# Kernel optimization log

Measured on AMD Instinct MI355X. Metric: run time of the kernel, lower is better.

## Reference

```python
import jax, jax.numpy as jnp
import numpy as np

B, N, DIM, H, DH = 2, 2048, 256, 8, 32
DIM_INNER = H * DH  # 256


def setup_inputs() -> dict:
    key = jax.random.key(0)
    ks = jax.random.split(key, 8)
    s = DIM ** -0.5  # keep activations / logits in a sane range
    return {
        "x_real": jax.random.normal(ks[0], (B, N, DIM), jnp.float32),
        "x_imag": jax.random.normal(ks[1], (B, N, DIM), jnp.float32),
        "wq_r": jax.random.normal(ks[2], (DIM, DIM_INNER), jnp.float32) * s,
        "wq_i": jax.random.normal(ks[3], (DIM, DIM_INNER), jnp.float32) * s,
        "wkv_r": jax.random.normal(ks[4], (DIM, 2 * DIM_INNER), jnp.float32) * s,
        "wkv_i": jax.random.normal(ks[5], (DIM, 2 * DIM_INNER), jnp.float32) * s,
        "wo_r": jax.random.normal(ks[6], (DIM_INNER, DIM), jnp.float32) * s,
        "wo_i": jax.random.normal(ks[7], (DIM_INNER, DIM), jnp.float32) * s,
    }


def _clin(xr, xi, wr, wi):
    # complex linear: (xr + i xi) @ (wr + i wi)
    return xr @ wr - xi @ wi, xr @ wi + xi @ wr


def _split_heads(t):
    b, n, _ = t.shape
    return t.reshape(b, n, H, DH).transpose(0, 2, 1, 3)  # b h n d


def _merge_heads(t):
    b, h, n, d = t.shape
    return t.transpose(0, 2, 1, 3).reshape(b, n, h * d)


def reference(x_real, x_imag, wq_r, wq_i, wkv_r, wkv_i, wo_r, wo_i):
    # complex projections
    qr, qi = _clin(x_real, x_imag, wq_r, wq_i)
    kvr, kvi = _clin(x_real, x_imag, wkv_r, wkv_i)
    kr, vr = jnp.split(kvr, 2, axis=-1)
    ki, vi = jnp.split(kvi, 2, axis=-1)
    qr, qi, kr, ki, vr, vi = map(_split_heads, (qr, qi, kr, ki, vr, vi))

    # complex_attention_complete (sec 3.2 eq 3): 4 real SDPA replicas.
    # q repeat '(c r b)' -> blocks [qr, qr, qi, qi]; k repeat '(r c b)' -> [kr, ki, kr, ki]
    scale = DH ** -0.5
    Q = jnp.stack([qr, qr, qi, qi])        # [4, b, h, n, d]
    K = jnp.stack([kr, ki, kr, ki])
    sim = jnp.einsum('rbhid,rbhjd->rbhij', Q, K) * scale
    A = jax.nn.softmax(sim, axis=-1)       # [4, b, h, n, n]

    av = lambda a, v: jnp.einsum('bhij,bhjd->bhid', a, v)
    # sign-recombine trick: indices [0,3,5,6 | 1,2,4,7], sign [[1,-1,-1,-1],[1,1,1,-1]]
    o_r = av(A[0], vr) - av(A[1], vi) - av(A[2], vi) - av(A[3], vr)
    o_i = av(A[0], vi) + av(A[1], vr) + av(A[2], vr) - av(A[3], vi)

    mr, mi = _merge_heads(o_r), _merge_heads(o_i)
    out_r, out_i = _clin(mr, mi, wo_r, wo_i)
    # real view of the complex output: [b, n, dim, 2]
    return jnp.stack([out_r, out_i], axis=-1)
```

## Files before the change

kernel.cpp:

```cpp
#include <hip/hip_runtime.h>
#include <math.h>

namespace {
constexpr int kB = 2, kN = 2048, kDim = 256, kH = 8, kDH = 32;
constexpr int kBH = kB * kH;
constexpr long kPlane = (long)kBH * kN * kDH;
constexpr float kQScaleL2 = 0.25506852552f;
}

typedef unsigned short u16;
typedef short short8 __attribute__((ext_vector_type(8)));
typedef short short4v __attribute__((ext_vector_type(4)));
typedef float floatx16 __attribute__((ext_vector_type(16)));
#define MFMA_BF16(a, b, c) __builtin_amdgcn_mfma_f32_32x32x16_bf16(a, b, c, 0, 0, 0)

__device__ inline u16 bf16b(float x) {
    union { float f; unsigned u; } c; c.f = x;
    unsigned r = c.u + 0x7FFFu + ((c.u >> 16) & 1u);
    return (u16)(r >> 16);
}
__device__ inline unsigned pack2(float x, float y) {
    return (unsigned)bf16b(x) | ((unsigned)bf16b(y) << 16);
}
__device__ inline unsigned packtr(float lo, float hi) {
    return __builtin_amdgcn_perm(__float_as_uint(hi), __float_as_uint(lo), 0x07060302u);
}
__device__ inline short8 mk8(const float* e) {
    union { unsigned u[4]; short8 s; } c;
    c.u[0] = packtr(e[0], e[1]);
    c.u[1] = packtr(e[2], e[3]);
    c.u[2] = packtr(e[4], e[5]);
    c.u[3] = packtr(e[6], e[7]);
    return c.s;
}
__device__ inline void gload16(const u16* g, u16* l) {
    __builtin_amdgcn_global_load_lds(
        (const __attribute__((address_space(1))) void*)g,
        (__attribute__((address_space(3))) void*)l, 16, 0, 0);
}

__global__ __launch_bounds__(256, 2) void prep_w(
    const float* __restrict__ xr_g, const float* __restrict__ xi_g,
    const float* __restrict__ wq_r, const float* __restrict__ wq_i,
    const float* __restrict__ wkv_r, const float* __restrict__ wkv_i,
    const float* __restrict__ wo_r, const float* __restrict__ wo_i,
    u16* __restrict__ Wbig, u16* __restrict__ WoT, u16* __restrict__ Xbf)
{
    const int T = blockIdx.x;
    const int tid = threadIdx.x;

    if (T < 256) {
        __shared__ __align__(16) u16 tile[64 * 68];
        const float* src;
        float sgn;
        int stride, colbase, kt, dt;
        bool isWo = false;
        int g = 0, ri = 0, hi;
        if (T < 192) {
            const int p = T >> 4, q = T & 15;
            kt = (q >> 2) * 64; dt = (q & 3) * 64;
            g = p >> 1; hi = p & 1;
            if (g < 2) {
                stride = 256; colbase = dt;
                if (g == 0) { src = hi ? wq_i : wq_r; sgn = hi ? -kQScaleL2 : kQScaleL2; }
                else        { src = hi ? wq_r : wq_i; sgn = kQScaleL2; }
            } else {
                stride = 512; colbase = dt + ((g >= 4) ? 256 : 0);
                if ((g & 1) == 0) { src = hi ? wkv_i : wkv_r; sgn = hi ? -1.f : 1.f; }
                else              { src = hi ? wkv_r : wkv_i; sgn = 1.f; }
            }
        } else {
            isWo = true;
            const int pp = T - 192;
            const int qd = pp >> 4, q = pp & 15;
            ri = qd & 1; hi = qd >> 1;
            kt = (q >> 2) * 64; dt = (q & 3) * 64;
            stride = 256; colbase = dt;
            if (ri == 0) { src = hi ? wo_i : wo_r; sgn = hi ? -1.f : 1.f; }
            else         { src = hi ? wo_r : wo_i; sgn = 1.f; }
        }

        const int ti = tid >> 4, tj = tid & 15;
        #pragma unroll
        for (int rr = 0; rr < 4; ++rr) {
            const int krel = ti + rr * 16;
            const float4 f = *(const float4*)(src + (long)(kt + krel) * stride
                                              + colbase + tj * 4);
            tile[(tj * 4 + 0) * 68 + krel] = bf16b(f.x * sgn);
            tile[(tj * 4 + 1) * 68 + krel] = bf16b(f.y * sgn);
            tile[(tj * 4 + 2) * 68 + krel] = bf16b(f.z * sgn);
            tile[(tj * 4 + 3) * 68 + krel] = bf16b(f.w * sgn);
        }
        __syncthreads();

        const int di = tid >> 4, kj = tid & 15;
        #pragma unroll
        for (int dr = 0; dr < 4; ++dr) {
            const int dd = di + dr * 16;
            const short4v v = *(const short4v*)(tile + dd * 68 + kj * 4);
            long idx;
            if (!isWo) idx = (long)(g * 256 + dt + dd) * 512 + hi * 256 + kt + kj * 4;
            else       idx = (long)(2 * (dt + dd) + ri) * 512 + hi * 256 + kt + kj * 4;
            *(short4v*)(((!isWo) ? Wbig : WoT) + idx) = v;
        }
    } else {
        const long o = ((long)(T - 256) * 256 + tid) * 4;
        const int row = (int)(o >> 9);
        const int col = (int)(o & 511);
        const float* src = (col < 256) ? (xr_g + (long)row * 256 + col)
                                       : (xi_g + (long)row * 256 + col - 256);
        const float4 f = *(const float4*)src;
        short4v v;
        v[0] = (short)bf16b(f.x); v[1] = (short)bf16b(f.y);
        v[2] = (short)bf16b(f.z); v[3] = (short)bf16b(f.w);
        *(short4v*)(Xbf + o) = v;
    }
}

__global__ __launch_bounds__(256, 2) void gemm_proj(
    const u16* __restrict__ Xbf, const u16* __restrict__ BT,
    u16* __restrict__ qr, u16* __restrict__ qi, u16* __restrict__ kr,
    u16* __restrict__ ki, u16* __restrict__ vrT, u16* __restrict__ viT)
{
    __shared__ __align__(16) u16 sA[2][128 * 32];
    __shared__ __align__(16) u16 sB[2][128 * 32];
    const int tid = threadIdx.x;
    const int lane = tid & 63, l31 = lane & 31, lh = lane >> 5;
    const int w = tid >> 6, wrow = w & 1, wcol = w >> 1;
    const int n0 = blockIdx.x * 128, m0 = blockIdx.y * 128;

    const int rb0 = w * 32;
    const int grow = lane >> 2;
    const int gseg = (lane & 3) * 8;

    auto stage = [&](int b, int kt) {
        #pragma unroll
        for (int half = 0; half < 2; ++half) {
            const int r = rb0 + half * 16;
            gload16(Xbf + (long)(m0 + r + grow) * 512 + kt + gseg, &sA[b][r * 32]);
            gload16(BT + (long)(n0 + r + grow) * 512 + kt + gseg, &sB[b][r * 32]);
        }
    };

    floatx16 a00 = {0}, a01 = {0}, a10 = {0}, a11 = {0};
    stage(0, 0);
    for (int it = 0; it < 16; ++it) {
        const int cur = it & 1;
        __syncthreads();
        if (it < 15) stage(cur ^ 1, (it + 1) * 32);
        #pragma unroll
        for (int s = 0; s < 2; ++s) {
            const int ko = s * 16 + lh * 8;
            const short8 fa0 = *(const short8*)(&sA[cur][(wrow * 64 + l31) * 32 + ko]);
            const short8 fa1 = *(const short8*)(&sA[cur][(wrow * 64 + 32 + l31) * 32 + ko]);
            const short8 fb0 = *(const short8*)(&sB[cur][(wcol * 64 + l31) * 32 + ko]);
            const short8 fb1 = *(const short8*)(&sB[cur][(wcol * 64 + 32 + l31) * 32 + ko]);
            a00 = MFMA_BF16(fa0, fb0, a00);
            a01 = MFMA_BF16(fa0, fb1, a01);
            a10 = MFMA_BF16(fa1, fb0, a10);
            a11 = MFMA_BF16(fa1, fb1, a11);
        }
    }

    __syncthreads();
    u16* scr = ((u16*)sA) + w * 1088;

    floatx16 accs[2][2] = {{a00, a01}, {a10, a11}};
    #pragma unroll
    for (int rt = 0; rt < 2; ++rt) {
        #pragma unroll
        for (int ct = 0; ct < 2; ++ct) {
            const int colb = n0 + wcol * 64 + ct * 32;
            const int g = colb >> 8;
            const int h = (colb & 255) >> 5;
            if (g < 4) {
                u16* pl = (g == 0) ? qr : (g == 1) ? qi : (g == 2) ? kr : ki;
                #pragma unroll
                for (int reg = 0; reg < 16; ++reg) {
                    const int row = m0 + wrow * 64 + rt * 32 + (reg & 3) + 8 * (reg >> 2) + 4 * lh;
                    const int b = row >> 11, nn = row & 2047;
                    pl[(((long)(b * 8 + h)) * 2048 + nn) * 32 + l31] = bf16b(accs[rt][ct][reg]);
                }
            } else {
                #pragma unroll
                for (int q = 0; q < 4; ++q) {
                    union { unsigned u[2]; uint2 v; } pk;
                    pk.u[0] = pack2(accs[rt][ct][4 * q + 0], accs[rt][ct][4 * q + 1]);
                    pk.u[1] = pack2(accs[rt][ct][4 * q + 2], accs[rt][ct][4 * q + 3]);
                    *(uint2*)(scr + l31 * 34 + 8 * q + 4 * lh) = pk.v;
                }
                asm volatile("s_waitcnt lgkmcnt(0)" ::: "memory");
                const int rowb = m0 + wrow * 64 + rt * 32;
                const int b_ = rowb >> 11, nnb = rowb & 2047;
                u16* plane = (g == 4) ? vrT : viT;
                u16* rowbase = plane + ((long)(b_ * 8 + h) * 32) * 2048 + nnb;
                const int p = lane & 15;
                const int sp = (p & ~6) | ((p & 2) << 1) | ((p & 4) >> 1);
                const int dgrp = lane >> 4;
                #pragma unroll
                for (int ds_ = 0; ds_ < 8; ++ds_) {
                    const int d = ds_ * 4 + dgrp;
                    const unsigned v = *(const unsigned*)(scr + d * 34 + 2 * sp);
                    *(unsigned*)(rowbase + (long)d * 2048 + 2 * p) = v;
                }
                asm volatile("s_waitcnt lgkmcnt(0)" ::: "memory");
            }
        }
    }
}

__global__ __launch_bounds__(256, 2) void attn_kernel(
    const u16* __restrict__ qr_g, const u16* __restrict__ qi_g,
    const u16* __restrict__ kr_g, const u16* __restrict__ ki_g,
    const u16* __restrict__ vrT_g, const u16* __restrict__ viT_g,
    u16* __restrict__ xo)
{
    __shared__ __align__(16) u16 smem[2][2][64 * 40];

    const int tid = threadIdx.x;
    const int lane = tid & 63, l31 = lane & 31, lh = lane >> 5;
    const int w = tid >> 6, strip = w & 1, qtype = w >> 1;
    const int bh = blockIdx.x;
    const int i0 = blockIdx.y * 64;
    const long base = (long)bh * kN * kDH;

    const u16* qg = (qtype ? qi_g : qr_g) + base;
    short8 qB0, qB1;
    {
        const u16* qp = qg + (long)(i0 + strip * 32 + l31) * kDH;
        qB0 = *(const short8*)(qp + lh * 8);
        qB1 = *(const short8*)(qp + 16 + lh * 8);
    }

    const int srow = tid & 63;
    const int sseg = tid >> 6;
    const u16* kptr = ((srow < 32) ? kr_g : ki_g) + base
                    + (long)(srow & 31) * kDH + sseg * 8;
    const u16* vptr = ((srow < 32) ? vrT_g : viT_g)
                    + ((long)bh * 32 + (srow & 31)) * kN + sseg * 8;

    short8 kreg = *(const short8*)kptr;
    short8 vreg = *(const short8*)vptr;

    floatx16 U0r = {0}, U0i = {0}, U1r = {0}, U1i = {0};
    float La0 = 0.f, La1 = 0.f;

    for (int t = 0; t < 64; ++t) {
        u16* bK = smem[0][t & 1];
        u16* bV = smem[1][t & 1];
        *(short8*)(bK + srow * 40 + sseg * 8) = kreg;
        *(short8*)(bV + srow * 40 + sseg * 8) = vreg;
        __syncthreads();
        if (t < 63) {
            kreg = *(const short8*)(kptr + (long)(t + 1) * 1024);
            vreg = *(const short8*)(vptr + (t + 1) * 32);
        }

        const short8 ka0 = *(const short8*)(bK + l31 * 40 + lh * 8);
        const short8 ka1 = *(const short8*)(bK + l31 * 40 + 16 + lh * 8);
        const short8 kb0 = *(const short8*)(bK + (32 + l31) * 40 + lh * 8);
        const short8 kb1 = *(const short8*)(bK + (32 + l31) * 40 + 16 + lh * 8);
        floatx16 S0 = {0}, S1 = {0};
        S0 = MFMA_BF16(ka0, qB0, S0);
        S0 = MFMA_BF16(ka1, qB1, S0);
        S1 = MFMA_BF16(kb0, qB0, S1);
        S1 = MFMA_BF16(kb1, qB1, S1);

        float e0[16], e1[16];
        #pragma unroll
        for (int r = 0; r < 16; ++r) {
            e0[r] = __builtin_amdgcn_exp2f(S0[r]);
            La0 += e0[r];
        }
        #pragma unroll
        for (int r = 0; r < 16; ++r) {
            e1[r] = __builtin_amdgcn_exp2f(S1[r]);
            La1 += e1[r];
        }
        const short8 F0a = mk8(&e0[0]);
        const short8 F0b = mk8(&e0[8]);
        const short8 F1a = mk8(&e1[0]);
        const short8 F1b = mk8(&e1[8]);

        const short8 va0 = *(const short8*)(bV + l31 * 40 + lh * 8);
        const short8 va1 = *(const short8*)(bV + l31 * 40 + 16 + lh * 8);
        const short8 vb0 = *(const short8*)(bV + (32 + l31) * 40 + lh * 8);
        const short8 vb1 = *(const short8*)(bV + (32 + l31) * 40 + 16 + lh * 8);

        U0r = MFMA_BF16(va0, F0a, U0r);
        U0r = MFMA_BF16(va1, F0b, U0r);
        U0i = MFMA_BF16(vb0, F0a, U0i);
        U0i = MFMA_BF16(vb1, F0b, U0i);
        U1r = MFMA_BF16(va0, F1a, U1r);
        U1r = MFMA_BF16(va1, F1b, U1r);
        U1i = MFMA_BF16(vb0, F1a, U1i);
        U1i = MFMA_BF16(vb1, F1b, U1i);
    }

    La0 += __shfl_xor(La0, 32);
    La1 += __shfl_xor(La1, 32);
    const float iL0 = 1.f / La0, iL1 = 1.f / La1;

    float po_r[16], po_i[16];
    #pragma unroll
    for (int r = 0; r < 16; ++r) {
        if (qtype == 0) {
            po_r[r] =  U0r[r] * iL0 - U1i[r] * iL1;
            po_i[r] =  U0i[r] * iL0 + U1r[r] * iL1;
        } else {
            po_r[r] = -U0i[r] * iL0 - U1r[r] * iL1;
            po_i[r] =  U0r[r] * iL0 - U1i[r] * iL1;
        }
    }

    __syncthreads();
    float* sC = (float*)smem;
    if (qtype == 1) {
        float* dst = sC + strip * (2 * 32 * 33);
        #pragma unroll
        for (int r = 0; r < 16; ++r) {
            const int d = (r & 3) + 8 * (r >> 2) + 4 * lh;
            dst[d * 33 + l31] = po_r[r];
            dst[32 * 33 + d * 33 + l31] = po_i[r];
        }
    }
    __syncthreads();
    if (qtype == 0) {
        const float* src = sC + strip * (2 * 32 * 33);
        const int b = bh >> 3, h = bh & 7;
        u16* xrow = xo + ((long)(b * 2048 + i0 + strip * 32 + l31)) * 512 + h * 32;
        #pragma unroll
        for (int g = 0; g < 4; ++g) {
            const int d0 = 8 * g + 4 * lh;
            union { unsigned u[2]; uint2 v; } pr, pi;
            pr.u[0] = pack2(po_r[4 * g + 0] + src[(d0 + 0) * 33 + l31],
                            po_r[4 * g + 1] + src[(d0 + 1) * 33 + l31]);
            pr.u[1] = pack2(po_r[4 * g + 2] + src[(d0 + 2) * 33 + l31],
                            po_r[4 * g + 3] + src[(d0 + 3) * 33 + l31]);
            pi.u[0] = pack2(po_i[4 * g + 0] + src[32 * 33 + (d0 + 0) * 33 + l31],
                            po_i[4 * g + 1] + src[32 * 33 + (d0 + 1) * 33 + l31]);
            pi.u[1] = pack2(po_i[4 * g + 2] + src[32 * 33 + (d0 + 2) * 33 + l31],
                            po_i[4 * g + 3] + src[32 * 33 + (d0 + 3) * 33 + l31]);
            *(uint2*)(xrow + d0) = pr.v;
            *(uint2*)(xrow + 256 + d0) = pi.v;
        }
    }
}

__global__ __launch_bounds__(256, 2) void gemm_oproj(
    const u16* __restrict__ Xo, const u16* __restrict__ BT, float* __restrict__ out)
{
    __shared__ __align__(16) u16 sA[2][64 * 32];
    __shared__ __align__(16) u16 sB[2][64 * 32];
    const int tid = threadIdx.x;
    const int lane = tid & 63, l31 = lane & 31, lh = lane >> 5;
    const int w = tid >> 6, wrow = w & 1, wcol = w >> 1;
    const int n0 = blockIdx.x * 64, m0 = blockIdx.y * 64;

    const int rb0 = w * 16;
    const int grow = lane >> 2;
    const int gseg = (lane & 3) * 8;

    auto stage = [&](int b, int kt) {
        gload16(Xo + (long)(m0 + rb0 + grow) * 512 + kt + gseg, &sA[b][rb0 * 32]);
        gload16(BT + (long)(n0 + rb0 + grow) * 512 + kt + gseg, &sB[b][rb0 * 32]);
    };

    floatx16 acc = {0};
    stage(0, 0);
    for (int it = 0; it < 16; ++it) {
        const int cur = it & 1;
        __syncthreads();
        if (it < 15) stage(cur ^ 1, (it + 1) * 32);
        #pragma unroll
        for (int s = 0; s < 2; ++s) {
            const int ko = s * 16 + lh * 8;
            const short8 fa = *(const short8*)(&sA[cur][(wrow * 32 + l31) * 32 + ko]);
            const short8 fb = *(const short8*)(&sB[cur][(wcol * 32 + l31) * 32 + ko]);
            acc = MFMA_BF16(fa, fb, acc);
        }
    }

    const int col = n0 + wcol * 32 + l31;
    #pragma unroll
    for (int reg = 0; reg < 16; ++reg) {
        const int row = m0 + wrow * 32 + (reg & 3) + 8 * (reg >> 2) + 4 * lh;
        out[(long)row * 512 + col] = acc[reg];
    }
}

extern "C" void kernel_launch(void* const* d_in, const int* in_sizes, int n_in,
                              void* d_out, int out_size, void* d_ws, size_t ws_size,
                              hipStream_t stream) {
    const float* xr    = (const float*)d_in[0];
    const float* xi    = (const float*)d_in[1];
    const float* wq_r  = (const float*)d_in[2];
    const float* wq_i  = (const float*)d_in[3];
    const float* wkv_r = (const float*)d_in[4];
    const float* wkv_i = (const float*)d_in[5];
    const float* wo_r  = (const float*)d_in[6];
    const float* wo_i  = (const float*)d_in[7];
    float* out = (float*)d_out;

    u16* ws16 = (u16*)d_ws;
    u16* qr   = ws16 + 0 * kPlane;
    u16* qi   = ws16 + 1 * kPlane;
    u16* kr   = ws16 + 2 * kPlane;
    u16* ki   = ws16 + 3 * kPlane;
    u16* vrT  = ws16 + 4 * kPlane;
    u16* viT  = ws16 + 5 * kPlane;
    u16* xo   = ws16 + 6 * kPlane;
    u16* Wbig = ws16 + 8 * kPlane;
    u16* WoT  = Wbig + 786432;
    u16* Xbf  = xo;

    prep_w<<<2304, 256, 0, stream>>>(xr, xi, wq_r, wq_i, wkv_r, wkv_i, wo_r, wo_i,
                                     Wbig, WoT, Xbf);
    gemm_proj<<<dim3(12, 32), 256, 0, stream>>>(Xbf, Wbig, qr, qi, kr, ki, vrT, viT);
    attn_kernel<<<dim3(kBH, kN / 64), 256, 0, stream>>>(qr, qi, kr, ki, vrT, viT, xo);
    gemm_oproj<<<dim3(8, 64), 256, 0, stream>>>(xo, WoT, out);
}
```

Measured before the change: 162.9 us.

## Software-pipeline PV MFMAs one iteration behind QK with triple-buffered V tiles

The P·V matrix multiplies for tile t-1 now issue right after the QK^T MFMAs of tile t, before that tile's exp2 work, so matrix-core and VALU work can overlap within a wave. V shared-memory tiles become triple-buffered so the previous tile's V is still intact while the next one is being written. A tail block after the loop handles the last tile's P·V. The cost is more shared memory and extra live registers for the carried probability fragments and V operands, which may put pressure on the two-blocks-per-CU occupancy target.

```diff
diff --git a/kernel.cpp b/kernel.cpp
--- a/kernel.cpp
+++ b/kernel.cpp
@@ -215,7 +215,7 @@
     const u16* __restrict__ vrT_g, const u16* __restrict__ viT_g,
     u16* __restrict__ xo)
 {
-    __shared__ __align__(16) u16 smem[2][2][64 * 40];
+    __shared__ __align__(16) u16 smem[5 * 2560];
 
     const int tid = threadIdx.x;
     const int lane = tid & 63, l31 = lane & 31, lh = lane >> 5;
@@ -244,16 +244,28 @@
 
     floatx16 U0r = {0}, U0i = {0}, U1r = {0}, U1i = {0};
     float La0 = 0.f, La1 = 0.f;
-
+    short8 pF0a, pF0b, pF1a, pF1b;
+
+    int vb = 0;
     for (int t = 0; t < 64; ++t) {
-        u16* bK = smem[0][t & 1];
-        u16* bV = smem[1][t & 1];
+        u16* bK = smem + (t & 1) * 2560;
+        u16* bV = smem + (2 + vb) * 2560;
+        const int vbp = vb ? vb - 1 : 2;
+        const u16* bVp = smem + (2 + vbp) * 2560;
         *(short8*)(bK + srow * 40 + sseg * 8) = kreg;
         *(short8*)(bV + srow * 40 + sseg * 8) = vreg;
         __syncthreads();
         if (t < 63) {
             kreg = *(const short8*)(kptr + (long)(t + 1) * 1024);
             vreg = *(const short8*)(vptr + (t + 1) * 32);
+        }
+
+        short8 va0, va1, vb0, vb1;
+        if (t) {
+            va0 = *(const short8*)(bVp + l31 * 40 + lh * 8);
+            va1 = *(const short8*)(bVp + l31 * 40 + 16 + lh * 8);
+            vb0 = *(const short8*)(bVp + (32 + l31) * 40 + lh * 8);
+            vb1 = *(const short8*)(bVp + (32 + l31) * 40 + 16 + lh * 8);
         }
 
         const short8 ka0 = *(const short8*)(bK + l31 * 40 + lh * 8);
@@ -266,6 +278,17 @@
         S1 = MFMA_BF16(kb0, qB0, S1);
         S1 = MFMA_BF16(kb1, qB1, S1);
 
+        if (t) {
+            U0r = MFMA_BF16(va0, pF0a, U0r);
+            U0r = MFMA_BF16(va1, pF0b, U0r);
+            U0i = MFMA_BF16(vb0, pF0a, U0i);
+            U0i = MFMA_BF16(vb1, pF0b, U0i);
+            U1r = MFMA_BF16(va0, pF1a, U1r);
+            U1r = MFMA_BF16(va1, pF1b, U1r);
+            U1i = MFMA_BF16(vb0, pF1a, U1i);
+            U1i = MFMA_BF16(vb1, pF1b, U1i);
+        }
+
         float e0[16], e1[16];
         #pragma unroll
         for (int r = 0; r < 16; ++r) {
@@ -277,24 +300,28 @@
             e1[r] = __builtin_amdgcn_exp2f(S1[r]);
             La1 += e1[r];
         }
-        const short8 F0a = mk8(&e0[0]);
-        const short8 F0b = mk8(&e0[8]);
-        const short8 F1a = mk8(&e1[0]);
-        const short8 F1b = mk8(&e1[8]);
-
-        const short8 va0 = *(const short8*)(bV + l31 * 40 + lh * 8);
-        const short8 va1 = *(const short8*)(bV + l31 * 40 + 16 + lh * 8);
-        const short8 vb0 = *(const short8*)(bV + (32 + l31) * 40 + lh * 8);
-        const short8 vb1 = *(const short8*)(bV + (32 + l31) * 40 + 16 + lh * 8);
-
-        U0r = MFMA_BF16(va0, F0a, U0r);
-        U0r = MFMA_BF16(va1, F0b, U0r);
-        U0i = MFMA_BF16(vb0, F0a, U0i);
-        U0i = MFMA_BF16(vb1, F0b, U0i);
-        U1r = MFMA_BF16(va0, F1a, U1r);
-        U1r = MFMA_BF16(va1, F1b, U1r);
-        U1i = MFMA_BF16(vb0, F1a, U1i);
-        U1i = MFMA_BF16(vb1, F1b, U1i);
+        pF0a = mk8(&e0[0]);
+        pF0b = mk8(&e0[8]);
+        pF1a = mk8(&e1[0]);
+        pF1b = mk8(&e1[8]);
+
+        vb = (vb == 2) ? 0 : vb + 1;
+    }
+
+    {
+        const u16* bVp = smem + 2 * 2560;
+        const short8 va0 = *(const short8*)(bVp + l31 * 40 + lh * 8);
+        const short8 va1 = *(const short8*)(bVp + l31 * 40 + 16 + lh * 8);
+        const short8 vb0 = *(const short8*)(bVp + (32 + l31) * 40 + lh * 8);
+        const short8 vb1 = *(const short8*)(bVp + (32 + l31) * 40 + 16 + lh * 8);
+        U0r = MFMA_BF16(va0, pF0a, U0r);
+        U0r = MFMA_BF16(va1, pF0b, U0r);
+        U0i = MFMA_BF16(vb0, pF0a, U0i);
+        U0i = MFMA_BF16(vb1, pF0b, U0i);
+        U1r = MFMA_BF16(va0, pF1a, U1r);
+        U1r = MFMA_BF16(va1, pF1b, U1r);
+        U1i = MFMA_BF16(vb0, pF1a, U1i);
+        U1i = MFMA_BF16(vb1, pF1b, U1i);
     }
 
     La0 += __shfl_xor(La0, 32);
```

Result: no change. 164.5 us (+1.0%).

## Process two query strips per wave in attention to reuse K/V fragments

Applied to the files above, without the earlier changes.

Each attention block now runs 2 waves instead of 4. Each wave handles both 32-row query strips, so the K and V fragments read from LDS are reused across two strips, and the staging loads per thread double. This halves the LDS fragment reads per unit of MFMA work and the number of barrier participants. The cost is roughly twice the accumulator registers per wave, which could lower occupancy or cause spills, and fewer waves are available per block to hide latency.

```diff
diff --git a/kernel.cpp b/kernel.cpp
--- a/kernel.cpp
+++ b/kernel.cpp
@@ -209,7 +209,7 @@
     }
 }
 
-__global__ __launch_bounds__(256, 2) void attn_kernel(
+__global__ __launch_bounds__(128, 2) void attn_kernel(
     const u16* __restrict__ qr_g, const u16* __restrict__ qi_g,
     const u16* __restrict__ kr_g, const u16* __restrict__ ki_g,
     const u16* __restrict__ vrT_g, const u16* __restrict__ viT_g,
@@ -219,130 +219,187 @@
 
     const int tid = threadIdx.x;
     const int lane = tid & 63, l31 = lane & 31, lh = lane >> 5;
-    const int w = tid >> 6, strip = w & 1, qtype = w >> 1;
+    const int qtype = tid >> 6;
     const int bh = blockIdx.x;
     const int i0 = blockIdx.y * 64;
     const long base = (long)bh * kN * kDH;
 
     const u16* qg = (qtype ? qi_g : qr_g) + base;
-    short8 qB0, qB1;
+    short8 qA0, qA1, qB0, qB1;
     {
-        const u16* qp = qg + (long)(i0 + strip * 32 + l31) * kDH;
-        qB0 = *(const short8*)(qp + lh * 8);
-        qB1 = *(const short8*)(qp + 16 + lh * 8);
+        const u16* qpA = qg + (long)(i0 + l31) * kDH;
+        qA0 = *(const short8*)(qpA + lh * 8);
+        qA1 = *(const short8*)(qpA + 16 + lh * 8);
+        const u16* qpB = qg + (long)(i0 + 32 + l31) * kDH;
+        qB0 = *(const short8*)(qpB + lh * 8);
+        qB1 = *(const short8*)(qpB + 16 + lh * 8);
     }
 
     const int srow = tid & 63;
-    const int sseg = tid >> 6;
+    const int sseg = (tid >> 6) * 16;
     const u16* kptr = ((srow < 32) ? kr_g : ki_g) + base
-                    + (long)(srow & 31) * kDH + sseg * 8;
+                    + (long)(srow & 31) * kDH + sseg;
     const u16* vptr = ((srow < 32) ? vrT_g : viT_g)
-                    + ((long)bh * 32 + (srow & 31)) * kN + sseg * 8;
-
-    short8 kreg = *(const short8*)kptr;
-    short8 vreg = *(const short8*)vptr;
-
-    floatx16 U0r = {0}, U0i = {0}, U1r = {0}, U1i = {0};
-    float La0 = 0.f, La1 = 0.f;
+                    + ((long)bh * 32 + (srow & 31)) * kN + sseg;
+
+    short8 k0 = *(const short8*)kptr;
+    short8 k1 = *(const short8*)(kptr + 8);
+    short8 v0 = *(const short8*)vptr;
+    short8 v1 = *(const short8*)(vptr + 8);
+
+    floatx16 UA0r = {0}, UA0i = {0}, UA1r = {0}, UA1i = {0};
+    floatx16 UB0r = {0}, UB0i = {0}, UB1r = {0}, UB1i = {0};
+    float LaA0 = 0.f, LaA1 = 0.f, LaB0 = 0.f, LaB1 = 0.f;
 
     for (int t = 0; t < 64; ++t) {
         u16* bK = smem[0][t & 1];
         u16* bV = smem[1][t & 1];
-        *(short8*)(bK + srow * 40 + sseg * 8) = kreg;
-        *(short8*)(bV + srow * 40 + sseg * 8) = vreg;
+        *(short8*)(bK + srow * 40 + sseg) = k0;
+        *(short8*)(bK + srow * 40 + sseg + 8) = k1;
+        *(short8*)(bV + srow * 40 + sseg) = v0;
+        *(short8*)(bV + srow * 40 + sseg + 8) = v1;
         __syncthreads();
         if (t < 63) {
-            kreg = *(const short8*)(kptr + (long)(t + 1) * 1024);
-            vreg = *(const short8*)(vptr + (t + 1) * 32);
+            k0 = *(const short8*)(kptr + (long)(t + 1) * 1024);
+            k1 = *(const short8*)(kptr + (long)(t + 1) * 1024 + 8);
+            v0 = *(const short8*)(vptr + (t + 1) * 32);
+            v1 = *(const short8*)(vptr + (t + 1) * 32 + 8);
         }
 
         const short8 ka0 = *(const short8*)(bK + l31 * 40 + lh * 8);
         const short8 ka1 = *(const short8*)(bK + l31 * 40 + 16 + lh * 8);
         const short8 kb0 = *(const short8*)(bK + (32 + l31) * 40 + lh * 8);
         const short8 kb1 = *(const short8*)(bK + (32 + l31) * 40 + 16 + lh * 8);
-        floatx16 S0 = {0}, S1 = {0};
-        S0 = MFMA_BF16(ka0, qB0, S0);
-        S0 = MFMA_BF16(ka1, qB1, S0);
-        S1 = MFMA_BF16(kb0, qB0, S1);
-        S1 = MFMA_BF16(kb1, qB1, S1);
-
-        float e0[16], e1[16];
-        #pragma unroll
-        for (int r = 0; r < 16; ++r) {
-            e0[r] = __builtin_amdgcn_exp2f(S0[r]);
-            La0 += e0[r];
-        }
-        #pragma unroll
-        for (int r = 0; r < 16; ++r) {
-            e1[r] = __builtin_amdgcn_exp2f(S1[r]);
-            La1 += e1[r];
-        }
-        const short8 F0a = mk8(&e0[0]);
-        const short8 F0b = mk8(&e0[8]);
-        const short8 F1a = mk8(&e1[0]);
-        const short8 F1b = mk8(&e1[8]);
+
+        short8 FA0a, FA0b, FA1a, FA1b;
+        {
+            floatx16 S0 = {0}, S1 = {0};
+            S0 = MFMA_BF16(ka0, qA0, S0);
+            S0 = MFMA_BF16(ka1, qA1, S0);
+            S1 = MFMA_BF16(kb0, qA0, S1);
+            S1 = MFMA_BF16(kb1, qA1, S1);
+            float e0[16], e1[16];
+            #pragma unroll
+            for (int r = 0; r < 16; ++r) {
+                e0[r] = __builtin_amdgcn_exp2f(S0[r]);
+                LaA0 += e0[r];
+            }
+            #pragma unroll
+            for (int r = 0; r < 16; ++r) {
+                e1[r] = __builtin_amdgcn_exp2f(S1[r]);
+                LaA1 += e1[r];
+            }
+            FA0a = mk8(&e0[0]); FA0b = mk8(&e0[8]);
+            FA1a = mk8(&e1[0]); FA1b = mk8(&e1[8]);
+        }
+
+        short8 FB0a, FB0b, FB1a, FB1b;
+        {
+            floatx16 S0 = {0}, S1 = {0};
+            S0 = MFMA_BF16(ka0, qB0, S0);
+            S0 = MFMA_BF16(ka1, qB1, S0);
+            S1 = MFMA_BF16(kb0, qB0, S1);
+            S1 = MFMA_BF16(kb1, qB1, S1);
+            float e0[16], e1[16];
+            #pragma unroll
+            for (int r = 0; r < 16; ++r) {
+                e0[r] = __builtin_amdgcn_exp2f(S0[r]);
+                LaB0 += e0[r];
+            }
+            #pragma unroll
+            for (int r = 0; r < 16; ++r) {
+                e1[r] = __builtin_amdgcn_exp2f(S1[r]);
+                LaB1 += e1[r];
+            }
+            FB0a = mk8(&e0[0]); FB0b = mk8(&e0[8]);
+            FB1a = mk8(&e1[0]); FB1b = mk8(&e1[8]);
+        }
 
         const short8 va0 = *(const short8*)(bV + l31 * 40 + lh * 8);
         const short8 va1 = *(const short8*)(bV + l31 * 40 + 16 + lh * 8);
         const short8 vb0 = *(const short8*)(bV + (32 + l31) * 40 + lh * 8);
         const short8 vb1 = *(const short8*)(bV + (32 + l31) * 40 + 16 + lh * 8);
 
-        U0r = MFMA_BF16(va0, F0a, U0r);
-        U0r = MFMA_BF16(va1, F0b, U0r);
-        U0i = MFMA_BF16(vb0, F0a, U0i);
-        U0i = MFMA_BF16(vb1, F0b, U0i);
-        U1r = MFMA_BF16(va0, F1a, U1r);
-        U1r = MFMA_BF16(va1, F1b, U1r);
-        U1i = MFMA_BF16(vb0, F1a, U1i);
-        U1i = MFMA_BF16(vb1, F1b, U1i);
-    }
-
-    La0 += __shfl_xor(La0, 32);
-    La1 += __shfl_xor(La1, 32);
-    const float iL0 = 1.f / La0, iL1 = 1.f / La1;
-
-    float po_r[16], po_i[16];
+        UA0r = MFMA_BF16(va0, FA0a, UA0r);
+        UA0r = MFMA_BF16(va1, FA0b, UA0r);
+        UA0i = MFMA_BF16(vb0, FA0a, UA0i);
+        UA0i = MFMA_BF16(vb1, FA0b, UA0i);
+        UA1r = MFMA_BF16(va0, FA1a, UA1r);
+        UA1r = MFMA_BF16(va1, FA1b, UA1r);
+        UA1i = MFMA_BF16(vb0, FA1a, UA1i);
+        UA1i = MFMA_BF16(vb1, FA1b, UA1i);
+
+        UB0r = MFMA_BF16(va0, FB0a, UB0r);
+        UB0r = MFMA_BF16(va1, FB0b, UB0r);
+        UB0i = MFMA_BF16(vb0, FB0a, UB0i);
+        UB0i = MFMA_BF16(vb1, FB0b, UB0i);
+        UB1r = MFMA_BF16(va0, FB1a, UB1r);
+        UB1r = MFMA_BF16(va1, FB1b, UB1r);
+        UB1i = MFMA_BF16(vb0, FB1a, UB1i);
+        UB1i = MFMA_BF16(vb1, FB1b, UB1i);
+    }
+
+    LaA0 += __shfl_xor(LaA0, 32);
+    LaA1 += __shfl_xor(LaA1, 32);
+    LaB0 += __shfl_xor(LaB0, 32);
+    LaB1 += __shfl_xor(LaB1, 32);
+    const float iA0 = 1.f / LaA0, iA1 = 1.f / LaA1;
+    const float iB0 = 1.f / LaB0, iB1 = 1.f / LaB1;
+
+    float pAr[16], pAi[16], pBr[16], pBi[16];
     #pragma unroll
     for (int r = 0; r < 16; ++r) {
         if (qtype == 0) {
-            po_r[r] =  U0r[r] * iL0 - U1i[r] * iL1;
-            po_i[r] =  U0i[r] * iL0 + U1r[r] * iL1;
+            pAr[r] =  UA0r[r] * iA0 - UA1i[r] * iA1;
+            pAi[r] =  UA0i[r] * iA0 + UA1r[r] * iA1;
+            pBr[r] =  UB0r[r] * iB0 - UB1i[r] * iB1;
+            pBi[r] =  UB0i[r] * iB0 + UB1r[r] * iB1;
         } else {
-            po_r[r] = -U0i[r] * iL0 - U1r[r] * iL1;
-            po_i[r] =  U0r[r] * iL0 - U1i[r] * iL1;
+            pAr[r] = -UA0i[r] * iA0 - UA1r[r] * iA1;
+            pAi[r] =  UA0r[r] * iA0 - UA1i[r] * iA1;
+            pBr[r] = -UB0i[r] * iB0 - UB1r[r] * iB1;
+            pBi[r] =  UB0r[r] * iB0 - UB1i[r] * iB1;
         }
     }
 
     __syncthreads();
     float* sC = (float*)smem;
     if (qtype == 1) {
-        float* dst = sC + strip * (2 * 32 * 33);
-        #pragma unroll
-        for (int r = 0; r < 16; ++r) {
-            const int d = (r & 3) + 8 * (r >> 2) + 4 * lh;
-            dst[d * 33 + l31] = po_r[r];
-            dst[32 * 33 + d * 33 + l31] = po_i[r];
+        #pragma unroll
+        for (int strip = 0; strip < 2; ++strip) {
+            float* dst = sC + strip * (2 * 32 * 33);
+            #pragma unroll
+            for (int r = 0; r < 16; ++r) {
+                const int d = (r & 3) + 8 * (r >> 2) + 4 * lh;
+                dst[d * 33 + l31] = strip ? pBr[r] : pAr[r];
+                dst[32 * 33 + d * 33 + l31] = strip ? pBi[r] : pAi[r];
+            }
         }
     }
     __syncthreads();
     if (qtype == 0) {
-        const float* src = sC + strip * (2 * 32 * 33);
         const int b = bh >> 3, h = bh & 7;
-        u16* xrow = xo + ((long)(b * 2048 + i0 + strip * 32 + l31)) * 512 + h * 32;
-        #pragma unroll
-        for (int g = 0; g < 4; ++g) {
-            const int d0 = 8 * g + 4 * lh;
-            union { unsigned u[2]; uint2 v; } pr, pi;
-            pr.u[0] = pack2(po_r[4 * g + 0] + src[(d0 + 0) * 33 + l31],
-                            po_r[4 * g + 1] + src[(d0 + 1) * 33 + l31]);
-            pr.u[1] = pack2(po_r[4 * g + 2] + src[(d0 + 2) * 33 + l31],
-                            po_r[4 * g + 3] + src[(d0 + 3) * 33 + l31]);
-            pi.u[0] = pack2(po_i[4 * g + 0] + src[32 * 33 + (d0 + 0) * 33 + l31],
-                            po_i[4 * g + 1] + src[32 * 33 + (d0 + 1) * 33 + l31]);
-            pi.u[1] = pack2(po_i[4 * g + 2] + src[32 * 33 + (d0 + 2) * 33 + l31],
-                            po_i[4 * g + 3] + src[32 * 33 + (d0 + 3) * 33 + l31]);
-            *(uint2*)(xrow + d0) = pr.v;
-            *(uint2*)(xrow + 256 + d0) = pi.v;
+        #pragma unroll
+        for (int strip = 0; strip < 2; ++strip) {
+            const float* src = sC + strip * (2 * 32 * 33);
+            const float* pr_ = strip ? pBr : pAr;
+            const float* pi_ = strip ? pBi : pAi;
+            u16* xrow = xo + ((long)(b * 2048 + i0 + strip * 32 + l31)) * 512 + h * 32;
+            #pragma unroll
+            for (int g = 0; g < 4; ++g) {
+                const int d0 = 8 * g + 4 * lh;
+                union { unsigned u[2]; uint2 v; } pr, pi;
+                pr.u[0] = pack2(pr_[4 * g + 0] + src[(d0 + 0) * 33 + l31],
+                                pr_[4 * g + 1] + src[(d0 + 1) * 33 + l31]);
+                pr.u[1] = pack2(pr_[4 * g + 2] + src[(d0 + 2) * 33 + l31],
+                                pr_[4 * g + 3] + src[(d0 + 3) * 33 + l31]);
+                pi.u[0] = pack2(pi_[4 * g + 0] + src[32 * 33 + (d0 + 0) * 33 + l31],
+                                pi_[4 * g + 1] + src[32 * 33 + (d0 + 1) * 33 + l31]);
+                pi.u[1] = pack2(pi_[4 * g + 2] + src[32 * 33 + (d0 + 2) * 33 + l31],
+                                pi_[4 * g + 3] + src[32 * 33 + (d0 + 3) * 33 + l31]);
+                *(uint2*)(xrow + d0) = pr.v;
+                *(uint2*)(xrow + 256 + d0) = pi.v;
+            }
         }
     }
 }
@@ -417,6 +474,6 @@
     prep_w<<<2304, 256, 0, stream>>>(xr, xi, wq_r, wq_i, wkv_r, wkv_i, wo_r, wo_i,
                                      Wbig, WoT, Xbf);
     gemm_proj<<<dim3(12, 32), 256, 0, stream>>>(Xbf, Wbig, qr, qi, kr, ki, vrT, viT);
-    attn_kernel<<<dim3(kBH, kN / 64), 256, 0, stream>>>(qr, qi, kr, ki, vrT, viT, xo);
+    attn_kernel<<<dim3(kBH, kN / 64), 128, 0, stream>>>(qr, qi, kr, ki, vrT, viT, xo);
     gemm_oproj<<<dim3(8, 64), 256, 0, stream>>>(xo, WoT, out);
 }
```

Result: slower. 264.6 us (+62.4%).
